# Optimization experiments

Measured on AMD Instinct MI355X. Metric: run time of the kernel, lower is better.

The kernel has to match this reference:

```python
import jax, jax.numpy as jnp
import numpy as np

N = 50000        # nodes
E = 600000       # edges
D = 128          # hidden dim
FID = 128        # fixed_input_dim (one-hot size)
RWSE = 16        # rwse_dim
G = 128          # num graphs
L = 4            # num GIN blocks
DEG = 1001       # degree embedding table (clamp to 1000)
GIN_EPS = 0.0
BN_EPS = 1e-5


def setup_inputs() -> dict:
    key = jax.random.key(0)
    ks = jax.random.split(key, 16)
    s = 0.05
    inp = {
        "feat_id": jax.random.randint(ks[0], (N,), 0, 100000),
        "edge_index": jax.random.randint(ks[1], (2, E), 0, N),
        "batch_idx": jnp.sort(jax.random.randint(ks[2], (N,), 0, G)),
        "rwse": jax.random.normal(ks[3], (N, RWSE), jnp.float32),
        "in_degrees": jax.random.randint(ks[4], (N,), 0, DEG),
        # parameters
        "value_W": jax.random.normal(ks[5], (FID, D), jnp.float32) * s,
        "value_b": jnp.zeros((D,), jnp.float32),
        "rwse_W": jax.random.normal(ks[6], (RWSE, D), jnp.float32) * s,
        "rwse_b": jnp.zeros((D,), jnp.float32),
        "deg_emb": jax.random.normal(ks[7], (DEG, D), jnp.float32) * s,
        "mlp_W1": jax.random.normal(ks[8], (L, D, D), jnp.float32) * s,
        "mlp_b1": jnp.zeros((L, D), jnp.float32),
        "mlp_W2": jax.random.normal(ks[9], (L, D, D), jnp.float32) * s,
        "mlp_b2": jnp.zeros((L, D), jnp.float32),
        "bn_gamma": 1.0 + jax.random.normal(ks[10], (L, D), jnp.float32) * s,
        "bn_beta": jax.random.normal(ks[11], (L, D), jnp.float32) * s,
        "bn_mean": jax.random.normal(ks[12], (L, D), jnp.float32) * s,
        "bn_var": 1.0 + jax.random.uniform(ks[13], (L, D), jnp.float32) * 0.1,
    }
    return inp


def reference(feat_id, edge_index, batch_idx, rwse, in_degrees,
              value_W, value_b, rwse_W, rwse_b, deg_emb,
              mlp_W1, mlp_b1, mlp_W2, mlp_b2,
              bn_gamma, bn_beta, bn_mean, bn_var):
    # one_hot(feat_id % FID) @ value_W  ==  row gather of value_W
    h_id = jnp.remainder(feat_id, FID)
    h_attr = value_W[h_id] + value_b                      # [N, D]
    h_attr = h_attr + rwse @ rwse_W + rwse_b              # rwse projection
    deg = jnp.clip(in_degrees, 0, DEG - 1)
    h = h_attr + deg_emb[deg]                             # [N, D]

    src, dst = edge_index[0], edge_index[1]
    for l in range(L):
        # GIN aggregation: sum of neighbor messages + (1+eps)*self
        agg = jax.ops.segment_sum(h[src], dst, num_segments=N)
        agg = agg + (1.0 + GIN_EPS) * h
        # MLP: Linear -> ReLU -> Linear
        m = jax.nn.relu(agg @ mlp_W1[l] + mlp_b1[l]) @ mlp_W2[l] + mlp_b2[l]
        # BatchNorm (inference stats) + ReLU
        inv = bn_gamma[l] * jax.lax.rsqrt(bn_var[l] + BN_EPS)
        h = jax.nn.relu((m - bn_mean[l]) * inv + bn_beta[l])

    # scatter-mean graph pooling
    pooled = jax.ops.segment_sum(h, batch_idx, num_segments=G)      # [G, D]
    count = jax.ops.segment_sum(jnp.ones((N, 1), h.dtype), batch_idx,
                                num_segments=G)                     # [G, 1]
    graph_feature = pooled / jnp.maximum(count, 1.0)
    return graph_feature, h
```

## Files before the change

kernel.cpp:

```cpp
#include <hip/hip_runtime.h>

#define N_NODES 50000
#define N_EDGES 600000
#define DIM 128
#define NGRAPH 128
#define NLAYER 4
#define BN_EPS 1e-5f
#define SCAN_BLK 1024
#define MROWS 64

#define EN_BLOCKS 25000
#define WT_BLOCKS 512
#define HB_BLOCKS 2344

using short8  = __attribute__((ext_vector_type(8))) short;
using float4v = __attribute__((ext_vector_type(4))) float;

__device__ __forceinline__ float bf2f(unsigned short u) {
    union { unsigned int i; float f; } c; c.i = ((unsigned int)u) << 16; return c.f;
}
__device__ __forceinline__ unsigned short f2bf(float f) {
    union { float f; unsigned int i; } c; c.f = f;
    unsigned int x = c.i;
    return (unsigned short)((x + 0x7fffu + ((x >> 16) & 1u)) >> 16);
}

__global__ void fused_pre_kernel(const int* __restrict__ feat_id,
                                 const float* __restrict__ rwse,
                                 const int* __restrict__ indeg,
                                 const float* __restrict__ value_W,
                                 const float* __restrict__ value_b,
                                 const float* __restrict__ rwse_W,
                                 const float* __restrict__ rwse_b,
                                 const float* __restrict__ deg_emb,
                                 unsigned short* __restrict__ hout,
                                 const float* __restrict__ W1,
                                 const float* __restrict__ W2,
                                 unsigned short* __restrict__ w1t,
                                 unsigned short* __restrict__ w2t,
                                 const int* __restrict__ dst,
                                 int* __restrict__ cnt)
{
    int b = blockIdx.x;
    if (b < EN_BLOCKS) {
        int idx = b * 256 + threadIdx.x;
        int n = idx >> 7, d = idx & 127;
        int fid = feat_id[n] & 127;
        float v = value_W[fid * DIM + d] + value_b[d] + rwse_b[d];
        const float* rr = rwse + n * 16;
        float acc = 0.f;
#pragma unroll
        for (int k = 0; k < 16; ++k) acc += rr[k] * rwse_W[k * DIM + d];
        v += acc;
        int dg = indeg[n]; dg = dg < 0 ? 0 : (dg > 1000 ? 1000 : dg);
        v += deg_emb[dg * DIM + d];
        hout[idx] = f2bf(v);
    } else if (b < EN_BLOCKS + WT_BLOCKS) {
        int idx = (b - EN_BLOCKS) * 256 + threadIdx.x;
        int i = idx & (DIM * DIM - 1);
        int l = (idx >> 14) & 3;
        int is2 = idx >= NLAYER * DIM * DIM;
        int n = i >> 7, k = i & 127;
        const float* W = (is2 ? W2 : W1) + l * DIM * DIM;
        unsigned short v = f2bf(W[k * DIM + n]);
        (is2 ? w2t : w1t)[l * DIM * DIM + n * DIM + k] = v;
    } else {
        int e = (b - EN_BLOCKS - WT_BLOCKS) * 256 + threadIdx.x;
        if (e < N_EDGES) atomicAdd(&cnt[dst[e]], 1);
    }
}

__global__ void scanA_kernel(const int* __restrict__ cnt, int* __restrict__ rp, int* __restrict__ bsum) {
    __shared__ int sc[SCAN_BLK];
    int t = threadIdx.x, i = blockIdx.x * SCAN_BLK + t;
    int v = (i < N_NODES) ? cnt[i] : 0;
    sc[t] = v; __syncthreads();
    for (int off = 1; off < SCAN_BLK; off <<= 1) {
        int add = (t >= off) ? sc[t - off] : 0;
        __syncthreads();
        sc[t] += add;
        __syncthreads();
    }
    if (i < N_NODES) rp[i] = sc[t] - v;
    if (t == SCAN_BLK - 1) bsum[blockIdx.x] = sc[t];
}

__global__ void scan_fixup_kernel(int* __restrict__ rp, const int* __restrict__ bsum,
                                  int* __restrict__ cur, int nsb) {
    __shared__ int sbx[64];
    int t = threadIdx.x;
    if (t < 64) {
        int v = (t < nsb) ? bsum[t] : 0;
        int orig = v;
        for (int off = 1; off < 64; off <<= 1) {
            int y = __shfl_up(v, off, 64);
            if (t >= off) v += y;
        }
        sbx[t] = v - orig;
    }
    __syncthreads();
    int i = blockIdx.x * 256 + t;
    if (i < N_NODES) { int v = rp[i] + sbx[i >> 10]; rp[i] = v; cur[i] = v; }
    else if (i == N_NODES) rp[i] = N_EDGES;
}

__global__ void scatter_kernel(const int* __restrict__ src, const int* __restrict__ dst,
                               int* __restrict__ cur, int* __restrict__ esrc) {
    int e = blockIdx.x * blockDim.x + threadIdx.x;
    if (e < N_EDGES) {
        int pos = atomicAdd(&cur[dst[e]], 1);
        esrc[pos] = src[e];
    }
}

__global__ void __launch_bounds__(256) agg_kernel(const unsigned short* __restrict__ hin,
                                                  const int* __restrict__ rp,
                                                  const int* __restrict__ esrc,
                                                  unsigned short* __restrict__ aggout)
{
    int node = (blockIdx.x * blockDim.x + threadIdx.x) >> 6;
    node = __builtin_amdgcn_readfirstlane(node);
    if (node >= N_NODES) return;
    int lane = threadIdx.x & 63;
    int grp = lane >> 4, q = lane & 15;

    float a[8];
    if (grp == 0) {
        uint4 s = *(const uint4*)(hin + (size_t)node * DIM + q * 8);
        a[0] = bf2f((unsigned short)(s.x & 0xffff)); a[1] = bf2f((unsigned short)(s.x >> 16));
        a[2] = bf2f((unsigned short)(s.y & 0xffff)); a[3] = bf2f((unsigned short)(s.y >> 16));
        a[4] = bf2f((unsigned short)(s.z & 0xffff)); a[5] = bf2f((unsigned short)(s.z >> 16));
        a[6] = bf2f((unsigned short)(s.w & 0xffff)); a[7] = bf2f((unsigned short)(s.w >> 16));
    } else {
#pragma unroll
        for (int i = 0; i < 8; ++i) a[i] = 0.f;
    }

    int e1 = rp[node + 1];
    int e = rp[node] + grp;
    int snext = (e < e1) ? esrc[e] : 0;
    while (e < e1) {
        int s = snext;
        int en = e + 4;
        snext = (en < e1) ? esrc[en] : 0;
        uint4 v = *(const uint4*)(hin + (size_t)s * DIM + q * 8);
        a[0] += bf2f((unsigned short)(v.x & 0xffff)); a[1] += bf2f((unsigned short)(v.x >> 16));
        a[2] += bf2f((unsigned short)(v.y & 0xffff)); a[3] += bf2f((unsigned short)(v.y >> 16));
        a[4] += bf2f((unsigned short)(v.z & 0xffff)); a[5] += bf2f((unsigned short)(v.z >> 16));
        a[6] += bf2f((unsigned short)(v.w & 0xffff)); a[7] += bf2f((unsigned short)(v.w >> 16));
        e = en;
    }

#pragma unroll
    for (int i = 0; i < 8; ++i) {
        a[i] += __shfl_xor(a[i], 16, 64);
        a[i] += __shfl_xor(a[i], 32, 64);
    }

    if (grp == 0) {
        uint4 o;
        o.x = (unsigned int)f2bf(a[0]) | ((unsigned int)f2bf(a[1]) << 16);
        o.y = (unsigned int)f2bf(a[2]) | ((unsigned int)f2bf(a[3]) << 16);
        o.z = (unsigned int)f2bf(a[4]) | ((unsigned int)f2bf(a[5]) << 16);
        o.w = (unsigned int)f2bf(a[6]) | ((unsigned int)f2bf(a[7]) << 16);
        *(uint4*)(aggout + (size_t)node * DIM + q * 8) = o;
    }
}

__global__ void __launch_bounds__(256, 3) mlp_kernel(
    const unsigned short* __restrict__ aggin,
    const unsigned short* __restrict__ w1t,
    const unsigned short* __restrict__ w2t,
    const float* __restrict__ b1, const float* __restrict__ b2,
    const float* __restrict__ gam, const float* __restrict__ bet,
    const float* __restrict__ mean, const float* __restrict__ var,
    unsigned short* __restrict__ hout, float* __restrict__ fout, int last)
{
    __shared__ unsigned short sA[MROWS * DIM];
    __shared__ unsigned short sW[DIM * DIM];
    const int tid = threadIdx.x;
    const int wave = tid >> 6, lane = tid & 63;
    const int fr = lane & 15, fg = lane >> 4;
    const int rowbase = blockIdx.x * MROWS;

    for (int i = tid * 8; i < DIM * DIM; i += 256 * 8) {
        short8 v = *(const short8*)(w1t + i);
        int n = i >> 7;
        int byte = i * 2; byte ^= (n & 7) << 4;
        *(short8*)((char*)sW + byte) = v;
    }
    for (int i = tid * 8; i < MROWS * DIM; i += 256 * 8) {
        int row = i >> 7;
        int node = rowbase + row;
        short8 v;
        if (node < N_NODES) v = *(const short8*)(aggin + (size_t)node * DIM + (i & 127));
        else { short z = 0; v = (short8){z,z,z,z,z,z,z,z}; }
        int byte = i * 2; byte ^= (row & 7) << 4;
        *(short8*)((char*)sA + byte) = v;
    }
    __syncthreads();

    float4v acc[8];
#pragma unroll
    for (int n = 0; n < 8; ++n) acc[n] = (float4v){0.f, 0.f, 0.f, 0.f};

#pragma unroll
    for (int ks = 0; ks < 4; ++ks) {
        int k0 = ks * 32 + fg * 8;
        short8 a0;
        { int row = wave * 16 + fr; int byte = row * 256 + k0 * 2; byte ^= (row & 7) << 4; a0 = *(const short8*)((char*)sA + byte); }
#pragma unroll
        for (int nb = 0; nb < 8; ++nb) {
            int col = nb * 16 + fr;
            int byte = col * 256 + k0 * 2; byte ^= (col & 7) << 4;
            short8 b = *(const short8*)((char*)sW + byte);
            acc[nb] = __builtin_amdgcn_mfma_f32_16x16x32_bf16(a0, b, acc[nb], 0, 0, 0);
        }
    }
    __syncthreads();

#pragma unroll
    for (int nb = 0; nb < 8; ++nb) {
        int col = nb * 16 + fr;
        float bias = b1[col];
#pragma unroll
        for (int r = 0; r < 4; ++r) {
            int row = wave * 16 + fg * 4 + r;
            float v = acc[nb][r] + bias;
            v = fmaxf(v, 0.f);
            int byte = row * 256 + col * 2; byte ^= (row & 7) << 4;
            *(unsigned short*)((char*)sA + byte) = f2bf(v);
        }
    }
    for (int i = tid * 8; i < DIM * DIM; i += 256 * 8) {
        short8 v = *(const short8*)(w2t + i);
        int n = i >> 7;
        int byte = i * 2; byte ^= (n & 7) << 4;
        *(short8*)((char*)sW + byte) = v;
    }
    __syncthreads();

    float4v acc2[8];
#pragma unroll
    for (int n = 0; n < 8; ++n) acc2[n] = (float4v){0.f, 0.f, 0.f, 0.f};

#pragma unroll
    for (int ks = 0; ks < 4; ++ks) {
        int k0 = ks * 32 + fg * 8;
        short8 a0;
        { int row = wave * 16 + fr; int byte = row * 256 + k0 * 2; byte ^= (row & 7) << 4; a0 = *(const short8*)((char*)sA + byte); }
#pragma unroll
        for (int nb = 0; nb < 8; ++nb) {
            int col = nb * 16 + fr;
            int byte = col * 256 + k0 * 2; byte ^= (col & 7) << 4;
            short8 b = *(const short8*)((char*)sW + byte);
            acc2[nb] = __builtin_amdgcn_mfma_f32_16x16x32_bf16(a0, b, acc2[nb], 0, 0, 0);
        }
    }

#pragma unroll
    for (int nb = 0; nb < 8; ++nb) {
        int col = nb * 16 + fr;
        float bias = b2[col];
        float iv = gam[col] * rsqrtf(var[col] + BN_EPS);
        float mn = mean[col], bt = bet[col];
#pragma unroll
        for (int r = 0; r < 4; ++r) {
            int row = wave * 16 + fg * 4 + r;
            int node = rowbase + row;
            if (node < N_NODES) {
                float v = acc2[nb][r] + bias;
                v = (v - mn) * iv + bt;
                v = fmaxf(v, 0.f);
                if (last) fout[(size_t)node * DIM + col] = v;
                else hout[(size_t)node * DIM + col] = f2bf(v);
            }
        }
    }
}

__global__ void __launch_bounds__(256) pool_partial_kernel(const float* __restrict__ h,
                                                           const int* __restrict__ batch,
                                                           float* __restrict__ partial)
{
    __shared__ float sums[256];
    __shared__ int sb[2];
    int g = blockIdx.x >> 3, split = blockIdx.x & 7;
    if (threadIdx.x < 2) {
        int target = g + threadIdx.x;
        int lo = 0, hi = N_NODES;
        while (lo < hi) { int mid = (lo + hi) >> 1; if (batch[mid] < target) lo = mid + 1; else hi = mid; }
        sb[threadIdx.x] = lo;
    }
    __syncthreads();
    int lo = sb[0], hi = sb[1];
    int d = threadIdx.x & 127, half = threadIdx.x >> 7;
    float acc = 0.f;
    for (int n = lo + split * 2 + half; n < hi; n += 16) acc += h[(size_t)n * DIM + d];
    sums[threadIdx.x] = acc;
    __syncthreads();
    if (threadIdx.x < 128)
        partial[blockIdx.x * DIM + threadIdx.x] = sums[threadIdx.x] + sums[threadIdx.x + 128];
}

__global__ void pool_comb_kernel(const float* __restrict__ partial,
                                 const int* __restrict__ batch,
                                 float* __restrict__ out)
{
    __shared__ int sb[2];
    int g = blockIdx.x, t = threadIdx.x;
    if (t < 2) {
        int target = g + t;
        int lo = 0, hi = N_NODES;
        while (lo < hi) { int mid = (lo + hi) >> 1; if (batch[mid] < target) lo = mid + 1; else hi = mid; }
        sb[t] = lo;
    }
    __syncthreads();
    float s = 0.f;
#pragma unroll
    for (int sp = 0; sp < 8; ++sp) s += partial[(g * 8 + sp) * DIM + t];
    float c = (float)(sb[1] - sb[0]);
    out[g * DIM + t] = s / fmaxf(c, 1.f);
}

extern "C" void kernel_launch(void* const* d_in, const int* in_sizes, int n_in,
                              void* d_out, int out_size, void* d_ws, size_t ws_size,
                              hipStream_t stream)
{
    const int*   feat_id = (const int*)d_in[0];
    const int*   eidx    = (const int*)d_in[1];
    const int*   batch   = (const int*)d_in[2];
    const float* rwse    = (const float*)d_in[3];
    const int*   indeg   = (const int*)d_in[4];
    const float* value_W = (const float*)d_in[5];
    const float* value_b = (const float*)d_in[6];
    const float* rwse_W  = (const float*)d_in[7];
    const float* rwse_b  = (const float*)d_in[8];
    const float* deg_emb = (const float*)d_in[9];
    const float* W1      = (const float*)d_in[10];
    const float* b1      = (const float*)d_in[11];
    const float* W2      = (const float*)d_in[12];
    const float* b2      = (const float*)d_in[13];
    const float* gam     = (const float*)d_in[14];
    const float* bet     = (const float*)d_in[15];
    const float* mean    = (const float*)d_in[16];
    const float* var     = (const float*)d_in[17];

    const int* srcv = eidx;
    const int* dstv = eidx + N_EDGES;

    char* p = (char*)d_ws;
    auto alloc = [&](size_t bytes) { char* r = p; p += (bytes + 255) & ~(size_t)255; return r; };
    unsigned short* hA   = (unsigned short*)alloc((size_t)N_NODES * DIM * 2);
    unsigned short* agg  = (unsigned short*)alloc((size_t)N_NODES * DIM * 2);
    int* cnt  = (int*)alloc((size_t)N_NODES * 4);
    int* rp   = (int*)alloc((size_t)(N_NODES + 1) * 4);
    int* cur  = (int*)alloc((size_t)N_NODES * 4);
    int* bsum = (int*)alloc(64 * 4);
    int* esrc = (int*)alloc((size_t)N_EDGES * 4);
    unsigned short* w1t = (unsigned short*)alloc((size_t)NLAYER * DIM * DIM * 2);
    unsigned short* w2t = (unsigned short*)alloc((size_t)NLAYER * DIM * DIM * 2);
    float* partial = (float*)alloc((size_t)NGRAPH * 8 * DIM * 4);

    float* out = (float*)d_out;
    float* hf  = out + NGRAPH * DIM;

    hipMemsetAsync(cnt, 0, (size_t)N_NODES * 4, stream);
    fused_pre_kernel<<<EN_BLOCKS + WT_BLOCKS + HB_BLOCKS, 256, 0, stream>>>(
        feat_id, rwse, indeg, value_W, value_b, rwse_W, rwse_b, deg_emb, hA,
        W1, W2, w1t, w2t, dstv, cnt);
    int nsb = (N_NODES + SCAN_BLK - 1) / SCAN_BLK;
    scanA_kernel<<<nsb, SCAN_BLK, 0, stream>>>(cnt, rp, bsum);
    scan_fixup_kernel<<<(N_NODES + 1 + 255) / 256, 256, 0, stream>>>(rp, bsum, cur, nsb);
    scatter_kernel<<<(N_EDGES + 255) / 256, 256, 0, stream>>>(srcv, dstv, cur, esrc);

    const int nrb = (N_NODES + MROWS - 1) / MROWS;
    for (int l = 0; l < NLAYER; ++l) {
        agg_kernel<<<(N_NODES * 64 + 255) / 256, 256, 0, stream>>>(hA, rp, esrc, agg);
        mlp_kernel<<<nrb, 256, 0, stream>>>(agg,
            w1t + l * DIM * DIM, w2t + l * DIM * DIM,
            b1 + l * DIM, b2 + l * DIM, gam + l * DIM, bet + l * DIM,
            mean + l * DIM, var + l * DIM,
            hA, hf, (l == NLAYER - 1) ? 1 : 0);
    }
    pool_partial_kernel<<<NGRAPH * 8, 256, 0, stream>>>(hf, batch, partial);
    pool_comb_kernel<<<NGRAPH, DIM, 0, stream>>>(partial, batch, out);
}
```

Baseline: 432.0 us.

## Restructure encoder, unroll gather by two, read MLP operands directly from global

The encoder now has each block handle 16 nodes, caching the rwse rows and indices in shared memory and holding the rwse weight column in registers, so far fewer blocks are launched. The neighbour-gather loop processes two edges per iteration so more loads are in flight. The MLP kernel drops shared-memory staging of the weights and the input tile, reading MFMA operands straight from global/L2. Only the hidden intermediate stays in LDS, and the occupancy hint rises to 4. The risk is more redundant global traffic for the weights across waves in exchange for less LDS use and fewer barriers.

```diff
diff --git a/kernel.cpp b/kernel.cpp
--- a/kernel.cpp
+++ b/kernel.cpp
@@ -9,7 +9,7 @@
 #define SCAN_BLK 1024
 #define MROWS 64
 
-#define EN_BLOCKS 25000
+#define EN_BLOCKS 3125
 #define WT_BLOCKS 512
 #define HB_BLOCKS 2344
 
@@ -43,18 +43,32 @@
 {
     int b = blockIdx.x;
     if (b < EN_BLOCKS) {
-        int idx = b * 256 + threadIdx.x;
-        int n = idx >> 7, d = idx & 127;
-        int fid = feat_id[n] & 127;
-        float v = value_W[fid * DIM + d] + value_b[d] + rwse_b[d];
-        const float* rr = rwse + n * 16;
-        float acc = 0.f;
-#pragma unroll
-        for (int k = 0; k < 16; ++k) acc += rr[k] * rwse_W[k * DIM + d];
-        v += acc;
-        int dg = indeg[n]; dg = dg < 0 ? 0 : (dg > 1000 ? 1000 : dg);
-        v += deg_emb[dg * DIM + d];
-        hout[idx] = f2bf(v);
+        __shared__ float srw[16][16];
+        __shared__ int   sfid[16], sdeg[16];
+        const int t = threadIdx.x;
+        const int base = b * 16;
+        srw[t >> 4][t & 15] = rwse[(size_t)base * 16 + t];
+        if (t < 16) sfid[t] = feat_id[base + t] & 127;
+        else if (t < 32) {
+            int dg = indeg[base + t - 16];
+            sdeg[t - 16] = dg < 0 ? 0 : (dg > 1000 ? 1000 : dg);
+        }
+        const int d = t & 127, half = t >> 7;
+        float wk[16];
+#pragma unroll
+        for (int k = 0; k < 16; ++k) wk[k] = rwse_W[k * DIM + d];
+        float vb = value_b[d] + rwse_b[d];
+        __syncthreads();
+#pragma unroll
+        for (int nn = 0; nn < 8; ++nn) {
+            int nl = half * 8 + nn;
+            int node = base + nl;
+            float v = value_W[sfid[nl] * DIM + d] + vb + deg_emb[sdeg[nl] * DIM + d];
+            float acc = 0.f;
+#pragma unroll
+            for (int k = 0; k < 16; ++k) acc += srw[nl][k] * wk[k];
+            hout[(size_t)node * DIM + d] = f2bf(v + acc);
+        }
     } else if (b < EN_BLOCKS + WT_BLOCKS) {
         int idx = (b - EN_BLOCKS) * 256 + threadIdx.x;
         int i = idx & (DIM * DIM - 1);
@@ -136,19 +150,28 @@
         for (int i = 0; i < 8; ++i) a[i] = 0.f;
     }
 
-    int e1 = rp[node + 1];
+    const int e1 = rp[node + 1];
     int e = rp[node] + grp;
-    int snext = (e < e1) ? esrc[e] : 0;
-    while (e < e1) {
-        int s = snext;
-        int en = e + 4;
-        snext = (en < e1) ? esrc[en] : 0;
-        uint4 v = *(const uint4*)(hin + (size_t)s * DIM + q * 8);
-        a[0] += bf2f((unsigned short)(v.x & 0xffff)); a[1] += bf2f((unsigned short)(v.x >> 16));
-        a[2] += bf2f((unsigned short)(v.y & 0xffff)); a[3] += bf2f((unsigned short)(v.y >> 16));
-        a[4] += bf2f((unsigned short)(v.z & 0xffff)); a[5] += bf2f((unsigned short)(v.z >> 16));
-        a[6] += bf2f((unsigned short)(v.w & 0xffff)); a[7] += bf2f((unsigned short)(v.w >> 16));
-        e = en;
+    bool p0 = e < e1, p1 = e + 4 < e1;
+    int s0 = p0 ? esrc[e] : 0;
+    int s1 = p1 ? esrc[e + 4] : 0;
+    while (p0) {
+        uint4 v0 = *(const uint4*)(hin + (size_t)s0 * DIM + q * 8);
+        uint4 v1;
+        if (p1) v1 = *(const uint4*)(hin + (size_t)s1 * DIM + q * 8);
+        else v1 = (uint4){0u, 0u, 0u, 0u};
+        e += 8;
+        p0 = e < e1; p1 = e + 4 < e1;
+        s0 = p0 ? esrc[e] : 0;
+        s1 = p1 ? esrc[e + 4] : 0;
+        a[0] += bf2f((unsigned short)(v0.x & 0xffff)) + bf2f((unsigned short)(v1.x & 0xffff));
+        a[1] += bf2f((unsigned short)(v0.x >> 16))    + bf2f((unsigned short)(v1.x >> 16));
+        a[2] += bf2f((unsigned short)(v0.y & 0xffff)) + bf2f((unsigned short)(v1.y & 0xffff));
+        a[3] += bf2f((unsigned short)(v0.y >> 16))    + bf2f((unsigned short)(v1.y >> 16));
+        a[4] += bf2f((unsigned short)(v0.z & 0xffff)) + bf2f((unsigned short)(v1.z & 0xffff));
+        a[5] += bf2f((unsigned short)(v0.z >> 16))    + bf2f((unsigned short)(v1.z >> 16));
+        a[6] += bf2f((unsigned short)(v0.w & 0xffff)) + bf2f((unsigned short)(v1.w & 0xffff));
+        a[7] += bf2f((unsigned short)(v0.w >> 16))    + bf2f((unsigned short)(v1.w >> 16));
     }
 
 #pragma unroll
@@ -167,7 +190,7 @@
     }
 }
 
-__global__ void __launch_bounds__(256, 3) mlp_kernel(
+__global__ void __launch_bounds__(256, 4) mlp_kernel(
     const unsigned short* __restrict__ aggin,
     const unsigned short* __restrict__ w1t,
     const unsigned short* __restrict__ w2t,
@@ -176,29 +199,15 @@
     const float* __restrict__ mean, const float* __restrict__ var,
     unsigned short* __restrict__ hout, float* __restrict__ fout, int last)
 {
-    __shared__ unsigned short sA[MROWS * DIM];
-    __shared__ unsigned short sW[DIM * DIM];
+    __shared__ unsigned short sM[MROWS * DIM];
     const int tid = threadIdx.x;
     const int wave = tid >> 6, lane = tid & 63;
     const int fr = lane & 15, fg = lane >> 4;
     const int rowbase = blockIdx.x * MROWS;
 
-    for (int i = tid * 8; i < DIM * DIM; i += 256 * 8) {
-        short8 v = *(const short8*)(w1t + i);
-        int n = i >> 7;
-        int byte = i * 2; byte ^= (n & 7) << 4;
-        *(short8*)((char*)sW + byte) = v;
-    }
-    for (int i = tid * 8; i < MROWS * DIM; i += 256 * 8) {
-        int row = i >> 7;
-        int node = rowbase + row;
-        short8 v;
-        if (node < N_NODES) v = *(const short8*)(aggin + (size_t)node * DIM + (i & 127));
-        else { short z = 0; v = (short8){z,z,z,z,z,z,z,z}; }
-        int byte = i * 2; byte ^= (row & 7) << 4;
-        *(short8*)((char*)sA + byte) = v;
-    }
-    __syncthreads();
+    int arow = rowbase + wave * 16 + fr;
+    if (arow >= N_NODES) arow = N_NODES - 1;
+    const unsigned short* aptr = aggin + (size_t)arow * DIM + fg * 8;
 
     float4v acc[8];
 #pragma unroll
@@ -206,18 +215,13 @@
 
 #pragma unroll
     for (int ks = 0; ks < 4; ++ks) {
-        int k0 = ks * 32 + fg * 8;
-        short8 a0;
-        { int row = wave * 16 + fr; int byte = row * 256 + k0 * 2; byte ^= (row & 7) << 4; a0 = *(const short8*)((char*)sA + byte); }
+        short8 a0 = *(const short8*)(aptr + ks * 32);
 #pragma unroll
         for (int nb = 0; nb < 8; ++nb) {
-            int col = nb * 16 + fr;
-            int byte = col * 256 + k0 * 2; byte ^= (col & 7) << 4;
-            short8 b = *(const short8*)((char*)sW + byte);
+            short8 b = *(const short8*)(w1t + (nb * 16 + fr) * DIM + ks * 32 + fg * 8);
             acc[nb] = __builtin_amdgcn_mfma_f32_16x16x32_bf16(a0, b, acc[nb], 0, 0, 0);
         }
     }
-    __syncthreads();
 
 #pragma unroll
     for (int nb = 0; nb < 8; ++nb) {
@@ -229,14 +233,8 @@
             float v = acc[nb][r] + bias;
             v = fmaxf(v, 0.f);
             int byte = row * 256 + col * 2; byte ^= (row & 7) << 4;
-            *(unsigned short*)((char*)sA + byte) = f2bf(v);
-        }
-    }
-    for (int i = tid * 8; i < DIM * DIM; i += 256 * 8) {
-        short8 v = *(const short8*)(w2t + i);
-        int n = i >> 7;
-        int byte = i * 2; byte ^= (n & 7) << 4;
-        *(short8*)((char*)sW + byte) = v;
+            *(unsigned short*)((char*)sM + byte) = f2bf(v);
+        }
     }
     __syncthreads();
 
@@ -248,12 +246,10 @@
     for (int ks = 0; ks < 4; ++ks) {
         int k0 = ks * 32 + fg * 8;
         short8 a0;
-        { int row = wave * 16 + fr; int byte = row * 256 + k0 * 2; byte ^= (row & 7) << 4; a0 = *(const short8*)((char*)sA + byte); }
+        { int row = wave * 16 + fr; int byte = row * 256 + k0 * 2; byte ^= (row & 7) << 4; a0 = *(const short8*)((char*)sM + byte); }
 #pragma unroll
         for (int nb = 0; nb < 8; ++nb) {
-            int col = nb * 16 + fr;
-            int byte = col * 256 + k0 * 2; byte ^= (col & 7) << 4;
-            short8 b = *(const short8*)((char*)sW + byte);
+            short8 b = *(const short8*)(w2t + (nb * 16 + fr) * DIM + k0);
             acc2[nb] = __builtin_amdgcn_mfma_f32_16x16x32_bf16(a0, b, acc2[nb], 0, 0, 0);
         }
     }
```

New measurement: 455.0 us. 1.05x slower.
